# Kernel optimization log

Hardware: AMD Instinct MI355X
Metric: run time of the kernel (lower is better)

The kernel has to match this reference:

```python
import jax, jax.numpy as jnp
import numpy as np


def gcn_conv(h, src, dst, n, W, b):
    # PyG GCNConv: linear, add self-loops, symmetric norm, scatter-sum, bias
    h = h @ W
    loop = jnp.arange(n)
    s = jnp.concatenate([src, loop])
    d = jnp.concatenate([dst, loop])
    deg = jax.ops.segment_sum(jnp.ones_like(d, h.dtype), d, num_segments=n)
    dinv = jnp.where(deg > 0, jax.lax.rsqrt(deg), 0.0)
    norm = dinv[s] * dinv[d]  # [E+N]
    out = jax.ops.segment_sum(h[s] * norm[:, None], d, num_segments=n)
    return out + b


def setup_inputs() -> dict:
    key = jax.random.key(0)
    ks = jax.random.split(key, 4)
    N, E, F_IN, F_H, F_OUT = 10000, 320000, 512, 128, 40
    x = jax.random.normal(ks[0], (N, F_IN), dtype=jnp.float32)
    edge_index = jax.random.randint(ks[1], (2, E), 0, N, dtype=jnp.int64)
    W1 = jax.random.normal(ks[2], (F_IN, F_H), dtype=jnp.float32) * (1.0 / np.sqrt(F_IN))
    b1 = jnp.zeros((F_H,), jnp.float32)
    W2 = jax.random.normal(ks[3], (F_H, F_OUT), dtype=jnp.float32) * (1.0 / np.sqrt(F_H))
    b2 = jnp.zeros((F_OUT,), jnp.float32)
    return {"x": x, "edge_index": edge_index, "W1": W1, "b1": b1, "W2": W2, "b2": b2}


def reference(x, edge_index, W1, b1, W2, b2):
    n = x.shape[0]
    src, dst = edge_index[0], edge_index[1]
    h = jax.nn.relu(gcn_conv(x, src, dst, n, W1, b1))
    logits = gcn_conv(h, src, dst, n, W2, b2)
    # regularizer: dense adjacency from edge list (duplicates summed), trace(L @ L)
    A = jnp.zeros((n, n), jnp.float32).at[src, dst].add(1.0)
    reg_loss = jnp.sum(A * A.T)  # == trace(A @ A)
    return jax.nn.log_softmax(logits, axis=1), reg_loss
```

## Files before the change

kernel.cpp:

```cpp
#include <hip/hip_runtime.h>
#include <hip/hip_bf16.h>


#define CAP 128

typedef __attribute__((ext_vector_type(8))) short short8;
typedef __attribute__((ext_vector_type(4))) float float4v;

__device__ __forceinline__ unsigned short f2bf(float f) {
    __hip_bfloat16 b = __float2bfloat16(f);
    return *reinterpret_cast<unsigned short*>(&b);
}
__device__ __forceinline__ float bf2f(unsigned short u) {
    __hip_bfloat16 b = *reinterpret_cast<__hip_bfloat16*>(&u);
    return __bfloat162float(b);
}

__global__ void k_prep(const float* __restrict__ x, unsigned short* __restrict__ xh, int total4,
                       const float* __restrict__ W1, unsigned short* __restrict__ Bh1,
                       unsigned short* __restrict__ Bl1,
                       const float* __restrict__ W2, unsigned short* __restrict__ Bh2,
                       unsigned short* __restrict__ Bl2,
                       int* __restrict__ zbase, int zints,
                       int convB, int p1B, int p2B) {
    int b = blockIdx.x;
    if (b < convB) {
        int i = b * 256 + threadIdx.x;
        if (i < total4) {
            float4 v = ((const float4*)x)[i];
            ushort4 h;
            h.x = f2bf(v.x); h.y = f2bf(v.y); h.z = f2bf(v.z); h.w = f2bf(v.w);
            ((ushort4*)xh)[i] = h;
        }
        return;
    }
    b -= convB;
    if (b < p1B) {
        int t = b * 256 + threadIdx.x;
        int lane = t & 63;
        int f = (t >> 6) % 8;
        int kb = (t >> 6) / 8;
        int kbase = kb * 32 + (lane >> 4) * 8;
        int n = f * 16 + (lane & 15);
        unsigned short hj[8], lj[8];
#pragma unroll
        for (int j = 0; j < 8; j++) {
            float v = W1[(size_t)(kbase + j) * 128 + n];
            unsigned short hb = f2bf(v);
            hj[j] = hb;
            lj[j] = f2bf(v - bf2f(hb));
        }
        ushort4 h0 = {hj[0], hj[1], hj[2], hj[3]}, h1 = {hj[4], hj[5], hj[6], hj[7]};
        ushort4 l0 = {lj[0], lj[1], lj[2], lj[3]}, l1 = {lj[4], lj[5], lj[6], lj[7]};
        ((ushort4*)Bh1)[t * 2] = h0; ((ushort4*)Bh1)[t * 2 + 1] = h1;
        ((ushort4*)Bl1)[t * 2] = l0; ((ushort4*)Bl1)[t * 2 + 1] = l1;
        return;
    }
    b -= p1B;
    if (b < p2B) {
        int t = b * 256 + threadIdx.x;
        if (t >= 4 * 3 * 64) return;
        int lane = t & 63;
        int f = (t >> 6) % 3;
        int kb = (t >> 6) / 3;
        int kbase = kb * 32 + (lane >> 4) * 8;
        int n = f * 16 + (lane & 15);
        unsigned short hj[8], lj[8];
#pragma unroll
        for (int j = 0; j < 8; j++) {
            float v = (n < 40) ? W2[(size_t)(kbase + j) * 40 + n] : 0.f;
            unsigned short hb = f2bf(v);
            hj[j] = hb;
            lj[j] = f2bf(v - bf2f(hb));
        }
        ushort4 h0 = {hj[0], hj[1], hj[2], hj[3]}, h1 = {hj[4], hj[5], hj[6], hj[7]};
        ushort4 l0 = {lj[0], lj[1], lj[2], lj[3]}, l1 = {lj[4], lj[5], lj[6], lj[7]};
        ((ushort4*)Bh2)[t * 2] = h0; ((ushort4*)Bh2)[t * 2 + 1] = h1;
        ((ushort4*)Bl2)[t * 2] = l0; ((ushort4*)Bl2)[t * 2 + 1] = l1;
        return;
    }
    b -= p2B;
    {
        int i = b * 256 + threadIdx.x;
        if (i < zints) zbase[i] = 0;
    }
}

__global__ void k_fill(const int* __restrict__ src, const int* __restrict__ dst, int E,
                       int* __restrict__ cnt, unsigned short* __restrict__ csr) {
    int e = blockIdx.x * blockDim.x + threadIdx.x;
    if (e >= E) return;
    int d = dst[e];
    int pos = atomicAdd(&cnt[d], 1);
    if (pos < CAP) csr[(size_t)d * CAP + pos] = (unsigned short)src[e];
}

template <int NF, int KB>
__global__ void k_mfma_gemm1(const unsigned short* __restrict__ Xh,
                             const unsigned short* __restrict__ Bh,
                             const unsigned short* __restrict__ Bl,
                             unsigned short* __restrict__ H0, int M) {
    const int K = KB * 32, N = NF * 16;
    int w = threadIdx.x >> 6, lane = threadIdx.x & 63;
    int m0 = blockIdx.x * 64 + w * 16;
    if (m0 >= M) return;
    float4v acc[NF] = {};
    const short8* A = (const short8*)(Xh + (size_t)(m0 + (lane & 15)) * K) + (lane >> 4);
    const short8* BH = ((const short8*)Bh) + lane;
    const short8* BL = ((const short8*)Bl) + lane;
    for (int kb = 0; kb < KB; kb++) {
        short8 a = A[kb * 4];
#pragma unroll
        for (int f = 0; f < NF; f++) {
            short8 bh = BH[(kb * NF + f) * 64];
            short8 bl = BL[(kb * NF + f) * 64];
            acc[f] = __builtin_amdgcn_mfma_f32_16x16x32_bf16(a, bh, acc[f], 0, 0, 0);
            acc[f] = __builtin_amdgcn_mfma_f32_16x16x32_bf16(a, bl, acc[f], 0, 0, 0);
        }
    }
    int row = (lane >> 4) * 4, col = lane & 15;
#pragma unroll
    for (int f = 0; f < NF; f++)
#pragma unroll
        for (int r = 0; r < 4; r++)
            H0[(size_t)(m0 + row + r) * N + f * 16 + col] = f2bf(acc[f][r]);
}

template <int NF, int KB>
__global__ void k_mfma_gemm2(const unsigned short* __restrict__ Ab,
                             const unsigned short* __restrict__ Bh,
                             const unsigned short* __restrict__ Bl,
                             float* __restrict__ LG, int M) {
    const int K = KB * 32, N = NF * 16;
    int w = threadIdx.x >> 6, lane = threadIdx.x & 63;
    int m0 = blockIdx.x * 64 + w * 16;
    if (m0 >= M) return;
    float4v acc[NF] = {};
    const short8* A = (const short8*)(Ab + (size_t)(m0 + (lane & 15)) * K) + (lane >> 4);
    const short8* BH = ((const short8*)Bh) + lane;
    const short8* BL = ((const short8*)Bl) + lane;
#pragma unroll
    for (int kb = 0; kb < KB; kb++) {
        short8 a = A[kb * 4];
#pragma unroll
        for (int f = 0; f < NF; f++) {
            short8 bh = BH[(kb * NF + f) * 64];
            short8 bl = BL[(kb * NF + f) * 64];
            acc[f] = __builtin_amdgcn_mfma_f32_16x16x32_bf16(a, bh, acc[f], 0, 0, 0);
            acc[f] = __builtin_amdgcn_mfma_f32_16x16x32_bf16(a, bl, acc[f], 0, 0, 0);
        }
    }
    int row = (lane >> 4) * 4, col = lane & 15;
#pragma unroll
    for (int f = 0; f < NF; f++)
#pragma unroll
        for (int r = 0; r < 4; r++)
            LG[(size_t)(m0 + row + r) * N + f * 16 + col] = acc[f][r];
}

__global__ void k_agg1_reg(const int* __restrict__ cnt, const unsigned short* __restrict__ csr,
                           const unsigned short* __restrict__ H, const float* __restrict__ b1,
                           unsigned* __restrict__ aggb,
                           const int* __restrict__ src, const int* __restrict__ dst, int E,
                           float* __restrict__ regp, int Nn, int aggBlocks) {
    if ((int)blockIdx.x < aggBlocks) {
        int wid = blockIdx.x * 4 + (threadIdx.x >> 6);
        int lane = threadIdx.x & 63;
        if (wid >= Nn) return;
        int len = min(cnt[wid], CAP);
        float dd = rsqrtf((float)len + 1.0f);
        const unsigned* H2 = (const unsigned*)H;
        unsigned ph = H2[(size_t)wid * 64 + lane];
        float sw = dd * dd;
        float accx = bf2f((unsigned short)(ph & 0xffff)) * sw;
        float accy = bf2f((unsigned short)(ph >> 16)) * sw;
        const unsigned short* row = csr + (size_t)wid * CAP;
        int j = 0;
        for (; j + 3 < len; j += 4) {
            int s0 = row[j], s1 = row[j + 1], s2 = row[j + 2], s3 = row[j + 3];
            float w0 = rsqrtf((float)cnt[s0] + 1.0f) * dd;
            float w1 = rsqrtf((float)cnt[s1] + 1.0f) * dd;
            float w2 = rsqrtf((float)cnt[s2] + 1.0f) * dd;
            float w3 = rsqrtf((float)cnt[s3] + 1.0f) * dd;
            unsigned p0 = H2[(size_t)s0 * 64 + lane];
            unsigned p1 = H2[(size_t)s1 * 64 + lane];
            unsigned p2 = H2[(size_t)s2 * 64 + lane];
            unsigned p3 = H2[(size_t)s3 * 64 + lane];
            accx += w0 * bf2f((unsigned short)(p0 & 0xffff)) + w1 * bf2f((unsigned short)(p1 & 0xffff));
            accy += w0 * bf2f((unsigned short)(p0 >> 16))   + w1 * bf2f((unsigned short)(p1 >> 16));
            accx += w2 * bf2f((unsigned short)(p2 & 0xffff)) + w3 * bf2f((unsigned short)(p3 & 0xffff));
            accy += w2 * bf2f((unsigned short)(p2 >> 16))   + w3 * bf2f((unsigned short)(p3 >> 16));
        }
        for (; j < len; j++) {
            int s0 = row[j];
            float w0 = rsqrtf((float)cnt[s0] + 1.0f) * dd;
            unsigned p0 = H2[(size_t)s0 * 64 + lane];
            accx += w0 * bf2f((unsigned short)(p0 & 0xffff));
            accy += w0 * bf2f((unsigned short)(p0 >> 16));
        }
        float2 bb = ((const float2*)b1)[lane];
        float vx = accx + bb.x, vy = accy + bb.y;
        vx = vx > 0.f ? vx : 0.f;
        vy = vy > 0.f ? vy : 0.f;
        aggb[(size_t)wid * 64 + lane] = (unsigned)f2bf(vx) | ((unsigned)f2bf(vy) << 16);
    } else {
        int e = ((int)blockIdx.x - aggBlocks) * 256 + (int)threadIdx.x;
        int c = 0;
        if (e < E) {
            int s = src[e];
            unsigned d = (unsigned)dst[e];
            int len = min(cnt[s], CAP);
            const unsigned short* row = csr + (size_t)s * CAP;
            for (int i = 0; i < len; i += 4) {
                uint2 v = *(const uint2*)(row + i);
                c += ((v.x & 0xffffu) == d) ? 1 : 0;
                c += ((v.x >> 16) == d && i + 1 < len) ? 1 : 0;
                c += ((v.y & 0xffffu) == d && i + 2 < len) ? 1 : 0;
                c += ((v.y >> 16) == d && i + 3 < len) ? 1 : 0;
            }
        }
#pragma unroll
        for (int off = 32; off; off >>= 1) c += __shfl_xor(c, off, 64);
        if ((threadIdx.x & 63) == 0 && c) atomicAdd(regp, (float)c);
    }
}

__global__ void k_agg2_lsm(const int* __restrict__ cnt, const unsigned short* __restrict__ csr,
                           const float* __restrict__ LG, const float* __restrict__ b2,
                           const float* __restrict__ regp, float* __restrict__ out,
                           int Nn, int F) {
    int wid = (blockIdx.x * blockDim.x + threadIdx.x) >> 6;
    int lane = threadIdx.x & 63;
    if (wid >= Nn) return;
    int len = min(cnt[wid], CAP);
    float dd = rsqrtf((float)len + 1.0f);
    bool act = lane < F;
    float acc = act ? LG[(size_t)wid * 48 + lane] * dd * dd : 0.f;
    const unsigned short* row = csr + (size_t)wid * CAP;
    int j = 0;
    for (; j + 3 < len; j += 4) {
        int s0 = row[j], s1 = row[j + 1], s2 = row[j + 2], s3 = row[j + 3];
        float w0 = rsqrtf((float)cnt[s0] + 1.0f) * dd;
        float w1 = rsqrtf((float)cnt[s1] + 1.0f) * dd;
        float w2 = rsqrtf((float)cnt[s2] + 1.0f) * dd;
        float w3 = rsqrtf((float)cnt[s3] + 1.0f) * dd;
        float a0 = act ? LG[(size_t)s0 * 48 + lane] : 0.f;
        float a1 = act ? LG[(size_t)s1 * 48 + lane] : 0.f;
        float a2 = act ? LG[(size_t)s2 * 48 + lane] : 0.f;
        float a3 = act ? LG[(size_t)s3 * 48 + lane] : 0.f;
        acc += w0 * a0 + w1 * a1 + w2 * a2 + w3 * a3;
    }
    for (; j < len; j++) {
        int s0 = row[j];
        float w0 = rsqrtf((float)cnt[s0] + 1.0f) * dd;
        float a0 = act ? LG[(size_t)s0 * 48 + lane] : 0.f;
        acc += w0 * a0;
    }
    float v = act ? acc + b2[lane] : -1e30f;
    float m = v;
#pragma unroll
    for (int off = 32; off; off >>= 1) m = fmaxf(m, __shfl_xor(m, off, 64));
    float ex = act ? expf(v - m) : 0.f;
    float ssum = ex;
#pragma unroll
    for (int off = 32; off; off >>= 1) ssum += __shfl_xor(ssum, off, 64);
    if (act) out[(size_t)wid * F + lane] = v - m - logf(ssum);
    if (wid == 0 && lane == 0) out[(size_t)Nn * F] = regp[0];
}

extern "C" void kernel_launch(void* const* d_in, const int* in_sizes, int n_in,
                              void* d_out, int out_size, void* d_ws, size_t ws_size,
                              hipStream_t stream) {
    const float* x  = (const float*)d_in[0];
    const int*   ei = (const int*)d_in[1];
    const float* W1 = (const float*)d_in[2];
    const float* b1 = (const float*)d_in[3];
    const float* W2 = (const float*)d_in[4];
    const float* b2 = (const float*)d_in[5];
    float* out = (float*)d_out;

    const int FH   = in_sizes[3];
    const int FOUT = in_sizes[5];
    const int FIN  = in_sizes[2] / FH;
    const int Nn   = in_sizes[0] / FIN;
    const int E    = in_sizes[1] / 2;
    const int* src = ei;
    const int* dst = ei + E;

    int*   cnt  = (int*)d_ws;
    float* regp = (float*)(cnt + Nn);
    unsigned short* csr   = (unsigned short*)(regp + 16);
    unsigned short* Xh    = csr + (size_t)Nn * CAP;
    unsigned short* H0b   = Xh + (size_t)Nn * FIN;
    unsigned short* AGG1b = H0b + (size_t)Nn * FH;
    unsigned short* Bh1   = AGG1b + (size_t)Nn * FH;
    unsigned short* Bl1   = Bh1 + 65536;
    unsigned short* Bh2   = Bl1 + 65536;
    unsigned short* Bl2   = Bh2 + 6144;
    float* LG0 = (float*)(Bl2 + 6144);

    int total4 = Nn * FIN / 4;
    int convB = (total4 + 255) / 256;
    int p1B = (16 * 8 * 64) / 256;
    int p2B = (4 * 3 * 64 + 255) / 256;
    int zints = Nn + 16;
    int zB = (zints + 255) / 256;
    k_prep<<<convB + p1B + p2B + zB, 256, 0, stream>>>(
        x, Xh, total4, W1, Bh1, Bl1, W2, Bh2, Bl2, cnt, zints, convB, p1B, p2B);

    k_fill<<<(E + 255) / 256, 256, 0, stream>>>(src, dst, E, cnt, csr);

    k_mfma_gemm1<8, 16><<<(Nn + 63) / 64, 256, 0, stream>>>(Xh, Bh1, Bl1, H0b, Nn);

    int aggBlocks = (Nn + 3) / 4;
    int regBlocks = (E + 255) / 256;
    k_agg1_reg<<<aggBlocks + regBlocks, 256, 0, stream>>>(
        cnt, csr, H0b, b1, (unsigned*)AGG1b, src, dst, E, regp, Nn, aggBlocks);

    k_mfma_gemm2<3, 4><<<(Nn + 63) / 64, 256, 0, stream>>>(AGG1b, Bh2, Bl2, LG0, Nn);

    k_agg2_lsm<<<(Nn * 64 + 255) / 256, 256, 0, stream>>>(cnt, csr, LG0, b2, regp, out, Nn, FOUT);
}
```

Baseline: 201.3 us.

## Fuse x conversion into GEMM1, merge CSR fill, widen gathers, store logits in bf16

GEMM1 now reads fp32 x directly and converts to bf16 in registers, which removes the separate conversion pass and the Xh buffer. The CSR fill runs as extra blocks in the same GEMM1 launch, saving one kernel launch. The aggregation loops use 128-bit index loads and batch 8 or 16 neighbour gathers, and the reg scan reads 8 indices per load. GEMM2 output is stored as bf16 to halve the gather traffic in agg2, at some cost in precision. Degree lookups are also clamped to CAP, which changes numerics when a node has more than CAP in-edges.

```diff
diff --git a/kernel.cpp b/kernel.cpp
--- a/kernel.cpp
+++ b/kernel.cpp
@@ -16,25 +16,12 @@
     return __bfloat162float(b);
 }
 
-__global__ void k_prep(const float* __restrict__ x, unsigned short* __restrict__ xh, int total4,
-                       const float* __restrict__ W1, unsigned short* __restrict__ Bh1,
+__global__ void k_prep(const float* __restrict__ W1, unsigned short* __restrict__ Bh1,
                        unsigned short* __restrict__ Bl1,
                        const float* __restrict__ W2, unsigned short* __restrict__ Bh2,
                        unsigned short* __restrict__ Bl2,
-                       int* __restrict__ zbase, int zints,
-                       int convB, int p1B, int p2B) {
+                       int* __restrict__ zbase, int zints, int p1B, int p2B) {
     int b = blockIdx.x;
-    if (b < convB) {
-        int i = b * 256 + threadIdx.x;
-        if (i < total4) {
-            float4 v = ((const float4*)x)[i];
-            ushort4 h;
-            h.x = f2bf(v.x); h.y = f2bf(v.y); h.z = f2bf(v.z); h.w = f2bf(v.w);
-            ((ushort4*)xh)[i] = h;
-        }
-        return;
-    }
-    b -= convB;
     if (b < p1B) {
         int t = b * 256 + threadIdx.x;
         int lane = t & 63;
@@ -86,30 +73,38 @@
     }
 }
 
-__global__ void k_fill(const int* __restrict__ src, const int* __restrict__ dst, int E,
-                       int* __restrict__ cnt, unsigned short* __restrict__ csr) {
-    int e = blockIdx.x * blockDim.x + threadIdx.x;
-    if (e >= E) return;
-    int d = dst[e];
-    int pos = atomicAdd(&cnt[d], 1);
-    if (pos < CAP) csr[(size_t)d * CAP + pos] = (unsigned short)src[e];
-}
-
 template <int NF, int KB>
-__global__ void k_mfma_gemm1(const unsigned short* __restrict__ Xh,
+__global__ void k_gemm1_fill(const float* __restrict__ X,
                              const unsigned short* __restrict__ Bh,
                              const unsigned short* __restrict__ Bl,
-                             unsigned short* __restrict__ H0, int M) {
+                             unsigned short* __restrict__ H0, int M,
+                             const int* __restrict__ src, const int* __restrict__ dst, int E,
+                             int* __restrict__ cnt, unsigned short* __restrict__ csr,
+                             int gemmBlocks) {
+    if ((int)blockIdx.x >= gemmBlocks) {
+        int e = ((int)blockIdx.x - gemmBlocks) * 256 + (int)threadIdx.x;
+        if (e >= E) return;
+        int d = dst[e];
+        int pos = atomicAdd(&cnt[d], 1);
+        if (pos < CAP) csr[(size_t)d * CAP + pos] = (unsigned short)src[e];
+        return;
+    }
     const int K = KB * 32, N = NF * 16;
     int w = threadIdx.x >> 6, lane = threadIdx.x & 63;
     int m0 = blockIdx.x * 64 + w * 16;
     if (m0 >= M) return;
     float4v acc[NF] = {};
-    const short8* A = (const short8*)(Xh + (size_t)(m0 + (lane & 15)) * K) + (lane >> 4);
+    const float* Arow = X + (size_t)(m0 + (lane & 15)) * K + (lane >> 4) * 8;
     const short8* BH = ((const short8*)Bh) + lane;
     const short8* BL = ((const short8*)Bl) + lane;
     for (int kb = 0; kb < KB; kb++) {
-        short8 a = A[kb * 4];
+        float4 f0 = *(const float4*)(Arow + kb * 32);
+        float4 f1 = *(const float4*)(Arow + kb * 32 + 4);
+        short8 a;
+        a[0] = (short)f2bf(f0.x); a[1] = (short)f2bf(f0.y);
+        a[2] = (short)f2bf(f0.z); a[3] = (short)f2bf(f0.w);
+        a[4] = (short)f2bf(f1.x); a[5] = (short)f2bf(f1.y);
+        a[6] = (short)f2bf(f1.z); a[7] = (short)f2bf(f1.w);
 #pragma unroll
         for (int f = 0; f < NF; f++) {
             short8 bh = BH[(kb * NF + f) * 64];
@@ -130,7 +125,7 @@
 __global__ void k_mfma_gemm2(const unsigned short* __restrict__ Ab,
                              const unsigned short* __restrict__ Bh,
                              const unsigned short* __restrict__ Bl,
-                             float* __restrict__ LG, int M) {
+                             unsigned short* __restrict__ LGb, int M) {
     const int K = KB * 32, N = NF * 16;
     int w = threadIdx.x >> 6, lane = threadIdx.x & 63;
     int m0 = blockIdx.x * 64 + w * 16;
@@ -155,7 +150,7 @@
     for (int f = 0; f < NF; f++)
 #pragma unroll
         for (int r = 0; r < 4; r++)
-            LG[(size_t)(m0 + row + r) * N + f * 16 + col] = acc[f][r];
+            LGb[(size_t)(m0 + row + r) * N + f * 16 + col] = f2bf(acc[f][r]);
 }
 
 __global__ void k_agg1_reg(const int* __restrict__ cnt, const unsigned short* __restrict__ csr,
@@ -176,24 +171,48 @@
         float accy = bf2f((unsigned short)(ph >> 16)) * sw;
         const unsigned short* row = csr + (size_t)wid * CAP;
         int j = 0;
-        for (; j + 3 < len; j += 4) {
-            int s0 = row[j], s1 = row[j + 1], s2 = row[j + 2], s3 = row[j + 3];
-            float w0 = rsqrtf((float)cnt[s0] + 1.0f) * dd;
-            float w1 = rsqrtf((float)cnt[s1] + 1.0f) * dd;
-            float w2 = rsqrtf((float)cnt[s2] + 1.0f) * dd;
-            float w3 = rsqrtf((float)cnt[s3] + 1.0f) * dd;
-            unsigned p0 = H2[(size_t)s0 * 64 + lane];
-            unsigned p1 = H2[(size_t)s1 * 64 + lane];
-            unsigned p2 = H2[(size_t)s2 * 64 + lane];
-            unsigned p3 = H2[(size_t)s3 * 64 + lane];
-            accx += w0 * bf2f((unsigned short)(p0 & 0xffff)) + w1 * bf2f((unsigned short)(p1 & 0xffff));
-            accy += w0 * bf2f((unsigned short)(p0 >> 16))   + w1 * bf2f((unsigned short)(p1 >> 16));
-            accx += w2 * bf2f((unsigned short)(p2 & 0xffff)) + w3 * bf2f((unsigned short)(p3 & 0xffff));
-            accy += w2 * bf2f((unsigned short)(p2 >> 16))   + w3 * bf2f((unsigned short)(p3 >> 16));
+        for (; j + 16 <= len; j += 16) {
+            uint4 iv0 = *(const uint4*)(row + j);
+            uint4 iv1 = *(const uint4*)(row + j + 8);
+            int s[16];
+            s[0] = iv0.x & 0xffff; s[1] = iv0.x >> 16; s[2] = iv0.y & 0xffff; s[3] = iv0.y >> 16;
+            s[4] = iv0.z & 0xffff; s[5] = iv0.z >> 16; s[6] = iv0.w & 0xffff; s[7] = iv0.w >> 16;
+            s[8] = iv1.x & 0xffff; s[9] = iv1.x >> 16; s[10] = iv1.y & 0xffff; s[11] = iv1.y >> 16;
+            s[12] = iv1.z & 0xffff; s[13] = iv1.z >> 16; s[14] = iv1.w & 0xffff; s[15] = iv1.w >> 16;
+            int cn[16];
+            unsigned p[16];
+#pragma unroll
+            for (int q = 0; q < 16; q++) cn[q] = cnt[s[q]];
+#pragma unroll
+            for (int q = 0; q < 16; q++) p[q] = H2[(size_t)s[q] * 64 + lane];
+#pragma unroll
+            for (int q = 0; q < 16; q++) {
+                float wq = rsqrtf((float)min(cn[q], CAP) + 1.0f) * dd;
+                accx += wq * bf2f((unsigned short)(p[q] & 0xffff));
+                accy += wq * bf2f((unsigned short)(p[q] >> 16));
+            }
+        }
+        for (; j + 8 <= len; j += 8) {
+            uint4 iv0 = *(const uint4*)(row + j);
+            int s[8];
+            s[0] = iv0.x & 0xffff; s[1] = iv0.x >> 16; s[2] = iv0.y & 0xffff; s[3] = iv0.y >> 16;
+            s[4] = iv0.z & 0xffff; s[5] = iv0.z >> 16; s[6] = iv0.w & 0xffff; s[7] = iv0.w >> 16;
+            int cn[8];
+            unsigned p[8];
+#pragma unroll
+            for (int q = 0; q < 8; q++) cn[q] = cnt[s[q]];
+#pragma unroll
+            for (int q = 0; q < 8; q++) p[q] = H2[(size_t)s[q] * 64 + lane];
+#pragma unroll
+            for (int q = 0; q < 8; q++) {
+                float wq = rsqrtf((float)min(cn[q], CAP) + 1.0f) * dd;
+                accx += wq * bf2f((unsigned short)(p[q] & 0xffff));
+                accy += wq * bf2f((unsigned short)(p[q] >> 16));
+            }
         }
         for (; j < len; j++) {
             int s0 = row[j];
-            float w0 = rsqrtf((float)cnt[s0] + 1.0f) * dd;
+            float w0 = rsqrtf((float)min(cnt[s0], CAP) + 1.0f) * dd;
             unsigned p0 = H2[(size_t)s0 * 64 + lane];
             accx += w0 * bf2f((unsigned short)(p0 & 0xffff));
             accy += w0 * bf2f((unsigned short)(p0 >> 16));
@@ -211,12 +230,16 @@
             unsigned d = (unsigned)dst[e];
             int len = min(cnt[s], CAP);
             const unsigned short* row = csr + (size_t)s * CAP;
-            for (int i = 0; i < len; i += 4) {
-                uint2 v = *(const uint2*)(row + i);
+            for (int i = 0; i < len; i += 8) {
+                uint4 v = *(const uint4*)(row + i);
                 c += ((v.x & 0xffffu) == d) ? 1 : 0;
                 c += ((v.x >> 16) == d && i + 1 < len) ? 1 : 0;
                 c += ((v.y & 0xffffu) == d && i + 2 < len) ? 1 : 0;
                 c += ((v.y >> 16) == d && i + 3 < len) ? 1 : 0;
+                c += ((v.z & 0xffffu) == d && i + 4 < len) ? 1 : 0;
+                c += ((v.z >> 16) == d && i + 5 < len) ? 1 : 0;
+                c += ((v.w & 0xffffu) == d && i + 6 < len) ? 1 : 0;
+                c += ((v.w >> 16) == d && i + 7 < len) ? 1 : 0;
             }
         }
 #pragma unroll
@@ -226,7 +249,7 @@
 }
 
 __global__ void k_agg2_lsm(const int* __restrict__ cnt, const unsigned short* __restrict__ csr,
-                           const float* __restrict__ LG, const float* __restrict__ b2,
+                           const unsigned short* __restrict__ LGb, const float* __restrict__ b2,
                            const float* __restrict__ regp, float* __restrict__ out,
                            int Nn, int F) {
     int wid = (blockIdx.x * blockDim.x + threadIdx.x) >> 6;
@@ -235,25 +258,30 @@
     int len = min(cnt[wid], CAP);
     float dd = rsqrtf((float)len + 1.0f);
     bool act = lane < F;
-    float acc = act ? LG[(size_t)wid * 48 + lane] * dd * dd : 0.f;
+    float acc = act ? bf2f(LGb[(size_t)wid * 48 + lane]) * dd * dd : 0.f;
     const unsigned short* row = csr + (size_t)wid * CAP;
     int j = 0;
-    for (; j + 3 < len; j += 4) {
-        int s0 = row[j], s1 = row[j + 1], s2 = row[j + 2], s3 = row[j + 3];
-        float w0 = rsqrtf((float)cnt[s0] + 1.0f) * dd;
-        float w1 = rsqrtf((float)cnt[s1] + 1.0f) * dd;
-        float w2 = rsqrtf((float)cnt[s2] + 1.0f) * dd;
-        float w3 = rsqrtf((float)cnt[s3] + 1.0f) * dd;
-        float a0 = act ? LG[(size_t)s0 * 48 + lane] : 0.f;
-        float a1 = act ? LG[(size_t)s1 * 48 + lane] : 0.f;
-        float a2 = act ? LG[(size_t)s2 * 48 + lane] : 0.f;
-        float a3 = act ? LG[(size_t)s3 * 48 + lane] : 0.f;
-        acc += w0 * a0 + w1 * a1 + w2 * a2 + w3 * a3;
+    for (; j + 8 <= len; j += 8) {
+        uint4 idv = *(const uint4*)(row + j);
+        int s[8];
+        s[0] = idv.x & 0xffff; s[1] = idv.x >> 16; s[2] = idv.y & 0xffff; s[3] = idv.y >> 16;
+        s[4] = idv.z & 0xffff; s[5] = idv.z >> 16; s[6] = idv.w & 0xffff; s[7] = idv.w >> 16;
+        int cn[8];
+        float a[8];
+#pragma unroll
+        for (int q = 0; q < 8; q++) cn[q] = cnt[s[q]];
+#pragma unroll
+        for (int q = 0; q < 8; q++) a[q] = act ? bf2f(LGb[(size_t)s[q] * 48 + lane]) : 0.f;
+#pragma unroll
+        for (int q = 0; q < 8; q++) {
+            float wq = rsqrtf((float)min(cn[q], CAP) + 1.0f) * dd;
+            acc += wq * a[q];
+        }
     }
     for (; j < len; j++) {
         int s0 = row[j];
-        float w0 = rsqrtf((float)cnt[s0] + 1.0f) * dd;
-        float a0 = act ? LG[(size_t)s0 * 48 + lane] : 0.f;
+        float w0 = rsqrtf((float)min(cnt[s0], CAP) + 1.0f) * dd;
+        float a0 = act ? bf2f(LGb[(size_t)s0 * 48 + lane]) : 0.f;
         acc += w0 * a0;
     }
     float v = act ? acc + b2[lane] : -1e30f;
@@ -290,34 +318,33 @@
     int*   cnt  = (int*)d_ws;
     float* regp = (float*)(cnt + Nn);
     unsigned short* csr   = (unsigned short*)(regp + 16);
-    unsigned short* Xh    = csr + (size_t)Nn * CAP;
-    unsigned short* H0b   = Xh + (size_t)Nn * FIN;
+    unsigned short* H0b   = csr + (size_t)Nn * CAP;
     unsigned short* AGG1b = H0b + (size_t)Nn * FH;
     unsigned short* Bh1   = AGG1b + (size_t)Nn * FH;
     unsigned short* Bl1   = Bh1 + 65536;
     unsigned short* Bh2   = Bl1 + 65536;
     unsigned short* Bl2   = Bh2 + 6144;
-    float* LG0 = (float*)(Bl2 + 6144);
-
-    int total4 = Nn * FIN / 4;
-    int convB = (total4 + 255) / 256;
+    unsigned short* LGb   = Bl2 + 6144;
+
     int p1B = (16 * 8 * 64) / 256;
     int p2B = (4 * 3 * 64 + 255) / 256;
     int zints = Nn + 16;
     int zB = (zints + 255) / 256;
-    k_prep<<<convB + p1B + p2B + zB, 256, 0, stream>>>(
-        x, Xh, total4, W1, Bh1, Bl1, W2, Bh2, Bl2, cnt, zints, convB, p1B, p2B);
-
-    k_fill<<<(E + 255) / 256, 256, 0, stream>>>(src, dst, E, cnt, csr);
-
-    k_mfma_gemm1<8, 16><<<(Nn + 63) / 64, 256, 0, stream>>>(Xh, Bh1, Bl1, H0b, Nn);
+    k_prep<<<p1B + p2B + zB, 256, 0, stream>>>(W1, Bh1, Bl1, W2, Bh2, Bl2,
+                                               cnt, zints, p1B, p2B);
+
+    int gemmB = (Nn + 63) / 64;
+    int fillB = (E + 255) / 256;
+    k_gemm1_fill<8, 16><<<gemmB + fillB, 256, 0, stream>>>(
+        x, Bh1, Bl1, H0b, Nn, src, dst, E, cnt, csr, gemmB);
 
     int aggBlocks = (Nn + 3) / 4;
     int regBlocks = (E + 255) / 256;
     k_agg1_reg<<<aggBlocks + regBlocks, 256, 0, stream>>>(
         cnt, csr, H0b, b1, (unsigned*)AGG1b, src, dst, E, regp, Nn, aggBlocks);
 
-    k_mfma_gemm2<3, 4><<<(Nn + 63) / 64, 256, 0, stream>>>(AGG1b, Bh2, Bl2, LG0, Nn);
-
-    k_agg2_lsm<<<(Nn * 64 + 255) / 256, 256, 0, stream>>>(cnt, csr, LG0, b2, regp, out, Nn, FOUT);
-}
+    k_mfma_gemm2<3, 4><<<(Nn + 63) / 64, 256, 0, stream>>>(AGG1b, Bh2, Bl2, LGb, Nn);
+
+    k_agg2_lsm<<<(Nn * 64 + 255) / 256, 256, 0, stream>>>(
+        cnt, csr, LGb, b2, regp, out, Nn, FOUT);
+}
```

Result: slower. 220.6 us (+9.6%).
